# Kernel tuning notes

Hardware: AMD Instinct MI355X
Metric: run time of the kernel (lower is better)

Reference implementation:

```python
import jax, jax.numpy as jnp
import numpy as np

FRAME_T = 8
NUM_K = 10


def _masked_att(att, temp):
    # att: [B, H, P, P] -> softmax over groups of size P//FRAME_T, top-k threshold mask
    B, H, P, _ = att.shape
    D = P // FRAME_T
    a = att.reshape(B, H, P, FRAME_T, D)
    a = jax.nn.softmax(a / temp, axis=-1)
    # k-th largest value per row as threshold (torch.topk values are sorted desc)
    margin = jax.lax.top_k(a, NUM_K)[0][..., -1]  # [B,H,P,FRAME_T]
    a = a * (a >= margin[..., None])
    return a  # [B,H,P,FRAME_T,D]


def setup_inputs() -> dict:
    key = jax.random.key(0)
    k1, k2, k3, k4 = jax.random.split(key, 4)
    B, H, P, hd = 4, 12, 1568, 64
    return {
        "att_s": jax.random.normal(k1, (B, H, P, P), dtype=jnp.float32),
        "att_t": jax.random.normal(k2, (B, H, P, P), dtype=jnp.float32),
        "v_s": jax.random.normal(k3, (B, H, P, hd), dtype=jnp.float32),
        "v_t": jax.random.normal(k4, (B, H, P, hd), dtype=jnp.float32),
    }


def reference(att_s, att_t, v_s, v_t):
    temp = jnp.float32(1.0)
    B, H, P, _ = att_t.shape
    H_s = att_s.shape[1]
    h_dim = v_t.shape[-1]
    D = P // FRAME_T

    a_s = _masked_att(att_s, temp)  # [B,Hs,P,T,D]
    a_t = _masked_att(att_t, temp)  # [B,H,P,T,D]

    vt = v_t.reshape(B, H, D, FRAME_T, h_dim)
    vs = v_s.reshape(B, H_s, D, FRAME_T, h_dim)

    norm_s = a_s.sum(-1)  # [B,Hs,P,T]
    norm_t = a_t.sum(-1)

    o_s = jnp.einsum('bhptd,bhdte->bhpte', a_s, vs) / norm_s[..., None]
    o_t = jnp.einsum('bhptd,bhdte->bhpte', a_t, vt) / norm_t[..., None]

    loss = jnp.mean((o_s - o_t) ** 2)
    return loss
```

## Files before the change

kernel.cpp:

```cpp
#include <hip/hip_runtime.h>
#include <hip/hip_bf16.h>

#define PP 1568
#define TT 8
#define DD 196
#define HD 64
#define NBH 48
#define NROW (NBH*PP*TT)
#define RPW 32
#define WPB 2
#define NWAVE (NROW/RPW)
#define NBLK5 (NWAVE/WPB)
#define NXCD 8
#define CPX (NBLK5/NXCD)
#define NPART NWAVE
#define NRED1 ((NPART+255)/256)
#define SUB (8*DD*4)
#define VSLAB (DD*TT*HD)
#define WPBH 392
#define KMASK 0xFFFFFF00u
#define NEG_INF (-3.0e38f)

typedef float f4 __attribute__((ext_vector_type(4)));
typedef unsigned u4v __attribute__((ext_vector_type(4)));

__device__ __forceinline__ float readlane_f(float v, int l) {
    return __int_as_float(__builtin_amdgcn_readlane(__float_as_int(v), l));
}

__device__ __forceinline__ float wave_sum_u(float v) {
#define STEPS(ctrl) { float t_ = __int_as_float(__builtin_amdgcn_update_dpp( \
        0, __float_as_int(v), ctrl, 0xF, 0xF, true)); v += t_; }
    STEPS(0x111) STEPS(0x112) STEPS(0x114) STEPS(0x118) STEPS(0x142) STEPS(0x143)
#undef STEPS
    return readlane_f(v, 63);
}

__device__ __forceinline__ float kval(float k) {
    return __uint_as_float(__float_as_uint(k) & KMASK);
}

struct K6  { float k0,k1,k2,k3,k4,k5; };
struct K10 { float k0,k1,k2,k3,k4,k5,k6,k7,k8,k9; };
struct MR  { K10 f; float mx; };

#define PUTK6(Q,X,D) { \
  unsigned cu_=(__float_as_uint(X)&KMASK)|(unsigned)(D); \
  float c_=__uint_as_float(cu_); \
  float n0_=fmaxf(Q.k0,c_); \
  float n1_=__builtin_amdgcn_fmed3f(Q.k0,Q.k1,c_); \
  float n2_=__builtin_amdgcn_fmed3f(Q.k1,Q.k2,c_); \
  float n3_=__builtin_amdgcn_fmed3f(Q.k2,Q.k3,c_); \
  float n4_=__builtin_amdgcn_fmed3f(Q.k3,Q.k4,c_); \
  float n5_=__builtin_amdgcn_fmed3f(Q.k4,Q.k5,c_); \
  Q.k0=n0_; Q.k1=n1_; Q.k2=n2_; Q.k3=n3_; Q.k4=n4_; Q.k5=n5_; }
#define PUT4K6(Q,V,D0) PUTK6(Q,(V).x,(D0)) PUTK6(Q,(V).y,(D0)+1) \
                       PUTK6(Q,(V).z,(D0)+2) PUTK6(Q,(V).w,(D0)+3)

__device__ __forceinline__ K6 chain_rows(const char* stg, int a, int b8) {
    K6 q = {NEG_INF,NEG_INF,NEG_INF,NEG_INF,NEG_INF,NEG_INF};
    const char* rb = stg + a*784 + b8*16;
    f4 v;
    v = *(const f4*)(rb);       PUT4K6(q, v, b8*4)
    v = *(const f4*)(rb+128);   PUT4K6(q, v, b8*4+32)
    v = *(const f4*)(rb+256);   PUT4K6(q, v, b8*4+64)
    v = *(const f4*)(rb+384);   PUT4K6(q, v, b8*4+96)
    v = *(const f4*)(rb+512);   PUT4K6(q, v, b8*4+128)
    v = *(const f4*)(rb+640);   PUT4K6(q, v, b8*4+160)
    if (b8 == 7) { f4 w = *(const f4*)(stg + a*784 + 768); PUT4K6(q, w, 192) }
    return q;
}

#define FSWZ(x, pat) __int_as_float(__builtin_amdgcn_ds_swizzle(__float_as_int(x), pat))
__device__ __forceinline__ K6 kshuf8_6(K6 a) {
    K6 r;
    r.k0=FSWZ(a.k0,0x201F); r.k1=FSWZ(a.k1,0x201F); r.k2=FSWZ(a.k2,0x201F);
    r.k3=FSWZ(a.k3,0x201F); r.k4=FSWZ(a.k4,0x201F); r.k5=FSWZ(a.k5,0x201F);
    return r;
}
__device__ __forceinline__ K10 kshuf16(K10 a) {
    K10 r;
    r.k0=FSWZ(a.k0,0x401F); r.k1=FSWZ(a.k1,0x401F); r.k2=FSWZ(a.k2,0x401F);
    r.k3=FSWZ(a.k3,0x401F); r.k4=FSWZ(a.k4,0x401F); r.k5=FSWZ(a.k5,0x401F);
    r.k6=FSWZ(a.k6,0x401F); r.k7=FSWZ(a.k7,0x401F); r.k8=FSWZ(a.k8,0x401F);
    r.k9=FSWZ(a.k9,0x401F);
    return r;
}
__device__ __forceinline__ float fbp(int bpx, float x) {
    return __int_as_float(__builtin_amdgcn_ds_bpermute(bpx, __float_as_int(x)));
}
__device__ __forceinline__ K10 kbp32(K10 a, int bpx) {
    K10 r;
    r.k0=fbp(bpx,a.k0); r.k1=fbp(bpx,a.k1); r.k2=fbp(bpx,a.k2);
    r.k3=fbp(bpx,a.k3); r.k4=fbp(bpx,a.k4); r.k5=fbp(bpx,a.k5);
    r.k6=fbp(bpx,a.k6); r.k7=fbp(bpx,a.k7); r.k8=fbp(bpx,a.k8);
    r.k9=fbp(bpx,a.k9);
    return r;
}

__device__ __forceinline__ K10 kmrg66(K6 A, K6 B) {
    float p00=fminf(A.k0,B.k0);
    float p01=fminf(A.k0,B.k1), p10=fminf(A.k1,B.k0);
    float p02=fminf(A.k0,B.k2), p11=fminf(A.k1,B.k1), p20=fminf(A.k2,B.k0);
    float p03=fminf(A.k0,B.k3), p12=fminf(A.k1,B.k2), p21=fminf(A.k2,B.k1), p30=fminf(A.k3,B.k0);
    float p04=fminf(A.k0,B.k4), p13=fminf(A.k1,B.k3), p22=fminf(A.k2,B.k2), p31=fminf(A.k3,B.k1), p40=fminf(A.k4,B.k0);
    float p05=fminf(A.k0,B.k5), p14=fminf(A.k1,B.k4), p23=fminf(A.k2,B.k3), p32=fminf(A.k3,B.k2), p41=fminf(A.k4,B.k1), p50=fminf(A.k5,B.k0);
    float p15=fminf(A.k1,B.k5), p24=fminf(A.k2,B.k4), p33=fminf(A.k3,B.k3), p42=fminf(A.k4,B.k2), p51=fminf(A.k5,B.k1);
    float p25=fminf(A.k2,B.k5), p34=fminf(A.k3,B.k4), p43=fminf(A.k4,B.k3), p52=fminf(A.k5,B.k2);
    float p35=fminf(A.k3,B.k5), p44=fminf(A.k4,B.k4), p53=fminf(A.k5,B.k3);
    K10 M;
    M.k0=fmaxf(A.k0,B.k0);
    M.k1=fmaxf(fmaxf(A.k1,B.k1),p00);
    M.k2=fmaxf(fmaxf(A.k2,B.k2),fmaxf(p01,p10));
    M.k3=fmaxf(fmaxf(A.k3,B.k3),fmaxf(p02,fmaxf(p11,p20)));
    M.k4=fmaxf(fmaxf(A.k4,B.k4),fmaxf(fmaxf(p03,p12),fmaxf(p21,p30)));
    M.k5=fmaxf(fmaxf(A.k5,B.k5),fmaxf(fmaxf(p04,p13),fmaxf(p22,fmaxf(p31,p40))));
    M.k6=fmaxf(fmaxf(p05,p14),fmaxf(fmaxf(p23,p32),fmaxf(p41,p50)));
    M.k7=fmaxf(fmaxf(p15,p24),fmaxf(p33,fmaxf(p42,p51)));
    M.k8=fmaxf(fmaxf(p25,p34),fmaxf(p43,p52));
    M.k9=fmaxf(p35,fmaxf(p44,p53));
    return M;
}

__device__ __forceinline__ K10 kmrg(K10 A, K10 B) {
    float p00=fminf(A.k0,B.k0);
    float p01=fminf(A.k0,B.k1), p10=fminf(A.k1,B.k0);
    float p02=fminf(A.k0,B.k2), p11=fminf(A.k1,B.k1), p20=fminf(A.k2,B.k0);
    float p03=fminf(A.k0,B.k3), p12=fminf(A.k1,B.k2), p21=fminf(A.k2,B.k1), p30=fminf(A.k3,B.k0);
    float p04=fminf(A.k0,B.k4), p13=fminf(A.k1,B.k3), p22=fminf(A.k2,B.k2), p31=fminf(A.k3,B.k1), p40=fminf(A.k4,B.k0);
    float p05=fminf(A.k0,B.k5), p14=fminf(A.k1,B.k4), p23=fminf(A.k2,B.k3), p32=fminf(A.k3,B.k2), p41=fminf(A.k4,B.k1), p50=fminf(A.k5,B.k0);
    float p06=fminf(A.k0,B.k6), p15=fminf(A.k1,B.k5), p24=fminf(A.k2,B.k4), p33=fminf(A.k3,B.k3), p42=fminf(A.k4,B.k2), p51=fminf(A.k5,B.k1), p60=fminf(A.k6,B.k0);
    float p07=fminf(A.k0,B.k7), p16=fminf(A.k1,B.k6), p25=fminf(A.k2,B.k5), p34=fminf(A.k3,B.k4), p43=fminf(A.k4,B.k3), p52=fminf(A.k5,B.k2), p61=fminf(A.k6,B.k1), p70=fminf(A.k7,B.k0);
    float p08=fminf(A.k0,B.k8), p17=fminf(A.k1,B.k7), p26=fminf(A.k2,B.k6), p35=fminf(A.k3,B.k5), p44=fminf(A.k4,B.k4), p53=fminf(A.k5,B.k3), p62=fminf(A.k6,B.k2), p71=fminf(A.k7,B.k1), p80=fminf(A.k8,B.k0);
    K10 M;
    M.k0=fmaxf(A.k0,B.k0);
    M.k1=fmaxf(fmaxf(A.k1,B.k1),p00);
    M.k2=fmaxf(fmaxf(A.k2,B.k2),fmaxf(p01,p10));
    M.k3=fmaxf(fmaxf(A.k3,B.k3),fmaxf(p02,fmaxf(p11,p20)));
    M.k4=fmaxf(fmaxf(A.k4,B.k4),fmaxf(fmaxf(p03,p12),fmaxf(p21,p30)));
    M.k5=fmaxf(fmaxf(A.k5,B.k5),fmaxf(fmaxf(p04,p13),fmaxf(p22,fmaxf(p31,p40))));
    M.k6=fmaxf(fmaxf(A.k6,B.k6),fmaxf(fmaxf(p05,p14),fmaxf(fmaxf(p23,p32),fmaxf(p41,p50))));
    M.k7=fmaxf(fmaxf(A.k7,B.k7),fmaxf(fmaxf(fmaxf(p06,p15),fmaxf(p24,p33)),fmaxf(fmaxf(p42,p51),p60)));
    M.k8=fmaxf(fmaxf(A.k8,B.k8),fmaxf(fmaxf(fmaxf(p07,p16),fmaxf(p25,p34)),fmaxf(fmaxf(p43,p52),fmaxf(p61,p70))));
    M.k9=fmaxf(fmaxf(A.k9,B.k9),fmaxf(fmaxf(fmaxf(p08,p17),fmaxf(p26,p35)),fmaxf(fmaxf(p44,p53),fmaxf(fmaxf(p62,p71),p80))));
    return M;
}

__device__ __forceinline__ MR merge_all(K6 q, int bpx) {
    K10 m = kmrg66(q, kshuf8_6(q));
    K10 n = kmrg(m, kshuf16(m));
    K10 r = kbp32(n, bpx);
    MR out;
    out.mx = fmaxf(n.k0, r.k0);
    out.f.k0=fmaxf(n.k0,r.k9); out.f.k1=fmaxf(n.k1,r.k8); out.f.k2=fmaxf(n.k2,r.k7);
    out.f.k3=fmaxf(n.k3,r.k6); out.f.k4=fmaxf(n.k4,r.k5); out.f.k5=fmaxf(n.k5,r.k4);
    out.f.k6=fmaxf(n.k6,r.k3); out.f.k7=fmaxf(n.k7,r.k2); out.f.k8=fmaxf(n.k8,r.k1);
    out.f.k9=fmaxf(n.k9,r.k0);
    return out;
}

#define LOADR(R, P) { const char* p_=(P); \
    R##0=*(const f4*)(p_+lane*16); \
    R##1=*(const f4*)(p_+1024+lane*16); \
    R##2=*(const f4*)(p_+2048+lane*16); \
    R##3=*(const f4*)(p_+3072+lane*16); \
    R##4=*(const f4*)(p_+4096+lane*16); \
    R##5=*(const f4*)(p_+5120+lane*16); \
    if (lane<8) R##6=*(const f4*)(p_+6144+lane*16); }
#define STORER(R) { \
    *(f4*)(stg+lane*16)=R##0; *(f4*)(stg+1024+lane*16)=R##1; \
    *(f4*)(stg+2048+lane*16)=R##2; *(f4*)(stg+3072+lane*16)=R##3; \
    *(f4*)(stg+4096+lane*16)=R##4; *(f4*)(stg+5120+lane*16)=R##5; \
    if (lane<8) *(f4*)(stg+6144+lane*16)=R##6; }

#define PKW(F,K) ((__float_as_uint(F)&KMASK)|(__float_as_uint(K)&0xFFu))

__global__ __launch_bounds__(128) void vtop_main(
        const float* __restrict__ att_s, const float* __restrict__ att_t,
        const float* __restrict__ v_s,   const float* __restrict__ v_t,
        float* __restrict__ partial) {
    __shared__ f4  stgv[WPB][SUB/16];
    __shared__ u4v wbuf[WPB][5][RPW];

    int tid  = threadIdx.x;
    int wid  = tid >> 6;
    int lane = tid & 63;
    char* stg = (char*)&stgv[wid][0];
    int a = lane & 7, b8 = lane >> 3;
    int bpx = (lane ^ 32) << 2;

    int blk = (blockIdx.x % NXCD) * CPX + blockIdx.x / NXCD;
    int gwave = blk * WPB + wid;
    int bh = gwave / WPBH;

    const char* baseS = (const char*)att_s + (size_t)gwave * (RPW*DD*4);
    const char* baseT = (const char*)att_t + (size_t)gwave * (RPW*DD*4);

    f4 rs0{},rs1{},rs2{},rs3{},rs4{},rs5{},rs6{};
    f4 rt0{},rt1{},rt2{},rt3{},rt4{},rt5{},rt6{};

    LOADR(rs, baseS)

#pragma unroll 1
    for (int s = 0; s < 4; ++s) {
        STORER(rs)
        LOADR(rt, baseT + s*SUB)
        K6 qS = chain_rows(stg, a, b8);
        MR mS = merge_all(qS, bpx);
        STORER(rt)
        if (s < 3) LOADR(rs, baseS + (s+1)*SUB)
        K6 qT = chain_rows(stg, a, b8);
        MR mT = merge_all(qT, bpx);
        K10 fS = mS.f, fT = mT.f;

        float CS = kval(mS.mx), CT = kval(mT.mx);
        float wS0=__expf(kval(fS.k0)-CS), wS1=__expf(kval(fS.k1)-CS),
              wS2=__expf(kval(fS.k2)-CS), wS3=__expf(kval(fS.k3)-CS),
              wS4=__expf(kval(fS.k4)-CS), wS5=__expf(kval(fS.k5)-CS),
              wS6=__expf(kval(fS.k6)-CS), wS7=__expf(kval(fS.k7)-CS),
              wS8=__expf(kval(fS.k8)-CS), wS9=__expf(kval(fS.k9)-CS);
        float wT0=__expf(kval(fT.k0)-CT), wT1=__expf(kval(fT.k1)-CT),
              wT2=__expf(kval(fT.k2)-CT), wT3=__expf(kval(fT.k3)-CT),
              wT4=__expf(kval(fT.k4)-CT), wT5=__expf(kval(fT.k5)-CT),
              wT6=__expf(kval(fT.k6)-CT), wT7=__expf(kval(fT.k7)-CT),
              wT8=__expf(kval(fT.k8)-CT), wT9=__expf(kval(fT.k9)-CT);
        float wsS = (((wS0+wS1)+(wS2+wS3))+((wS4+wS5)+(wS6+wS7)))+(wS8+wS9);
        float wsT = (((wT0+wT1)+(wT2+wT3))+((wT4+wT5)+(wT6+wT7)))+(wT8+wT9);
        float invS =  __builtin_amdgcn_rcpf(wsS);
        float invT = -__builtin_amdgcn_rcpf(wsT);

        if (lane < 8) {
            int row = (s << 3) | lane;
            u4v w;
            w.x=PKW(wS0*invS,fS.k0); w.y=PKW(wS1*invS,fS.k1);
            w.z=PKW(wS2*invS,fS.k2); w.w=PKW(wS3*invS,fS.k3);
            wbuf[wid][0][row]=w;
            w.x=PKW(wS4*invS,fS.k4); w.y=PKW(wS5*invS,fS.k5);
            w.z=PKW(wS6*invS,fS.k6); w.w=PKW(wS7*invS,fS.k7);
            wbuf[wid][1][row]=w;
            w.x=PKW(wS8*invS,fS.k8); w.y=PKW(wS9*invS,fS.k9);
            w.z=PKW(wT0*invT,fT.k0); w.w=PKW(wT1*invT,fT.k1);
            wbuf[wid][2][row]=w;
            w.x=PKW(wT2*invT,fT.k2); w.y=PKW(wT3*invT,fT.k3);
            w.z=PKW(wT4*invT,fT.k4); w.w=PKW(wT5*invT,fT.k5);
            wbuf[wid][3][row]=w;
            w.x=PKW(wT6*invT,fT.k6); w.y=PKW(wT7*invT,fT.k7);
            w.z=PKW(wT8*invT,fT.k8); w.w=PKW(wT9*invT,fT.k9);
            wbuf[wid][4][row]=w;
        }
    }

    const float* vSb = v_s + (size_t)bh * VSLAB;
    const float* vTb = v_t + (size_t)bh * VSLAB;
    unsigned ul = (unsigned)lane;
    float lacc = 0.f;
#pragma unroll 1
    for (int k = 0; k < RPW; ++k) {
        unsigned t64 = ((unsigned)(k & 7) << 6);
        const float* vSk = vSb + t64;
        const float* vTk = vTb + t64;
        u4v w0v=wbuf[wid][0][k], w1v=wbuf[wid][1][k], w2v=wbuf[wid][2][k],
            w3v=wbuf[wid][3][k], w4v=wbuf[wid][4][k];
        float d0=0.f, d1=0.f, d2=0.f, d3=0.f;
#define TRM(U, VB, ACC) { unsigned pk_=(unsigned)__builtin_amdgcn_readfirstlane((int)(U)); \
        float wf_ = __uint_as_float(pk_ & KMASK); \
        ACC = fmaf(wf_, VB[((pk_ & 0xFFu) << 9) + ul], ACC); }
        TRM(w0v.x, vSk, d0) TRM(w0v.y, vSk, d1) TRM(w0v.z, vSk, d2) TRM(w0v.w, vSk, d3)
        TRM(w1v.x, vSk, d0) TRM(w1v.y, vSk, d1) TRM(w1v.z, vSk, d2) TRM(w1v.w, vSk, d3)
        TRM(w2v.x, vSk, d0) TRM(w2v.y, vSk, d1)
        TRM(w2v.z, vTk, d2) TRM(w2v.w, vTk, d3)
        TRM(w3v.x, vTk, d0) TRM(w3v.y, vTk, d1) TRM(w3v.z, vTk, d2) TRM(w3v.w, vTk, d3)
        TRM(w4v.x, vTk, d0) TRM(w4v.y, vTk, d1) TRM(w4v.z, vTk, d2) TRM(w4v.w, vTk, d3)
#undef TRM
        float dsum = (d0 + d1) + (d2 + d3);
        lacc = fmaf(dsum, dsum, lacc);
    }

    float tot = wave_sum_u(lacc);
    if (lane == 0) partial[gwave] = tot;
}

__global__ __launch_bounds__(256) void vtop_reduce1(
        const float* __restrict__ partial, float* __restrict__ p2) {
    int i = blockIdx.x * 256 + threadIdx.x;
    float v = (i < NPART) ? partial[i] : 0.f;
    float wtot = wave_sum_u(v);
    __shared__ float sm[4];
    int lane = threadIdx.x & 63, wid = threadIdx.x >> 6;
    if (lane == 0) sm[wid] = wtot;
    __syncthreads();
    if (threadIdx.x == 0) p2[blockIdx.x] = (sm[0] + sm[1]) + (sm[2] + sm[3]);
}

__global__ __launch_bounds__(256) void vtop_reduce2(
        const float* __restrict__ p2, float* __restrict__ out) {
    __shared__ double smd[256];
    double a = 0.0;
    if (threadIdx.x < NRED1) a = (double)p2[threadIdx.x];
    smd[threadIdx.x] = a;
    __syncthreads();
    for (int s = 128; s > 0; s >>= 1) {
        if (threadIdx.x < s) smd[threadIdx.x] += smd[threadIdx.x + s];
        __syncthreads();
    }
    if (threadIdx.x == 0) {
        const double inv_n = 1.0 / ((double)NBH * PP * TT * HD);
        out[0] = (float)(smd[0] * inv_n);
    }
}

extern "C" void kernel_launch(void* const* d_in, const int* in_sizes, int n_in,
                              void* d_out, int out_size, void* d_ws, size_t ws_size,
                              hipStream_t stream) {
    const float* att_s = (const float*)d_in[0];
    const float* att_t = (const float*)d_in[1];
    const float* v_s   = (const float*)d_in[2];
    const float* v_t   = (const float*)d_in[3];
    float* out     = (float*)d_out;
    float* partial = (float*)d_ws;
    float* p2      = (float*)d_ws + NPART;

    vtop_main<<<NBLK5, 128, 0, stream>>>(att_s, att_t, v_s, v_t, partial);
    vtop_reduce1<<<NRED1, 256, 0, stream>>>(partial, p2);
    vtop_reduce2<<<1, 256, 0, stream>>>(p2, out);
}
```

Baseline: 323.7 us.

## Stage attention rows with direct global-to-LDS loads instead of register copies

Replaces the register-held prefetch of each row block (global load into VGPRs, then store to LDS) with `global_load_lds` builtins that write straight into the per-wave staging buffer. A `vmcnt(0)` wait precedes each read of the buffer. The loop is reordered so the S-side softmax weights are computed while the T-side block is in flight, and the next S block is issued after the T rows are read. This drops the register round trip and 28 f4 prefetch registers, which may help occupancy. In exchange only one block is in flight at a time, and overwriting the single buffer right after `chain_rows` relies on the LDS reads finishing before the async writes land.

```diff
diff --git a/kernel.cpp b/kernel.cpp
--- a/kernel.cpp
+++ b/kernel.cpp
@@ -38,6 +38,12 @@
 
 __device__ __forceinline__ float kval(float k) {
     return __uint_as_float(__float_as_uint(k) & KMASK);
+}
+
+__device__ __forceinline__ void gload_lds(const void* g, void* l) {
+    __builtin_amdgcn_global_load_lds(
+        (const __attribute__((address_space(1))) unsigned*)g,
+        (__attribute__((address_space(3))) unsigned*)l, 16, 0, 0);
 }
 
 struct K6  { float k0,k1,k2,k3,k4,k5; };
@@ -159,19 +165,15 @@
     return out;
 }
 
-#define LOADR(R, P) { const char* p_=(P); \
-    R##0=*(const f4*)(p_+lane*16); \
-    R##1=*(const f4*)(p_+1024+lane*16); \
-    R##2=*(const f4*)(p_+2048+lane*16); \
-    R##3=*(const f4*)(p_+3072+lane*16); \
-    R##4=*(const f4*)(p_+4096+lane*16); \
-    R##5=*(const f4*)(p_+5120+lane*16); \
-    if (lane<8) R##6=*(const f4*)(p_+6144+lane*16); }
-#define STORER(R) { \
-    *(f4*)(stg+lane*16)=R##0; *(f4*)(stg+1024+lane*16)=R##1; \
-    *(f4*)(stg+2048+lane*16)=R##2; *(f4*)(stg+3072+lane*16)=R##3; \
-    *(f4*)(stg+4096+lane*16)=R##4; *(f4*)(stg+5120+lane*16)=R##5; \
-    if (lane<8) *(f4*)(stg+6144+lane*16)=R##6; }
+#define STAGE(SRC) { const char* s_=(SRC); \
+    gload_lds(s_ +         (size_t)lane*16, stg); \
+    gload_lds(s_ + 1024 +  (size_t)lane*16, stg+1024); \
+    gload_lds(s_ + 2048 +  (size_t)lane*16, stg+2048); \
+    gload_lds(s_ + 3072 +  (size_t)lane*16, stg+3072); \
+    gload_lds(s_ + 4096 +  (size_t)lane*16, stg+4096); \
+    gload_lds(s_ + 5120 +  (size_t)lane*16, stg+5120); \
+    if (lane < 8) gload_lds(s_ + 6144 + (size_t)lane*16, stg+6144); }
+#define WAITV asm volatile("s_waitcnt vmcnt(0)" ::: "memory");
 
 #define PKW(F,K) ((__float_as_uint(F)&KMASK)|(__float_as_uint(K)&0xFFu))
 
@@ -196,37 +198,36 @@
     const char* baseS = (const char*)att_s + (size_t)gwave * (RPW*DD*4);
     const char* baseT = (const char*)att_t + (size_t)gwave * (RPW*DD*4);
 
-    f4 rs0{},rs1{},rs2{},rs3{},rs4{},rs5{},rs6{};
-    f4 rt0{},rt1{},rt2{},rt3{},rt4{},rt5{},rt6{};
-
-    LOADR(rs, baseS)
+    STAGE(baseS)
 
 #pragma unroll 1
     for (int s = 0; s < 4; ++s) {
-        STORER(rs)
-        LOADR(rt, baseT + s*SUB)
+        WAITV
         K6 qS = chain_rows(stg, a, b8);
+        STAGE(baseT + s*SUB)
         MR mS = merge_all(qS, bpx);
-        STORER(rt)
-        if (s < 3) LOADR(rs, baseS + (s+1)*SUB)
-        K6 qT = chain_rows(stg, a, b8);
-        MR mT = merge_all(qT, bpx);
-        K10 fS = mS.f, fT = mT.f;
-
-        float CS = kval(mS.mx), CT = kval(mT.mx);
+        K10 fS = mS.f;
+        float CS = kval(mS.mx);
         float wS0=__expf(kval(fS.k0)-CS), wS1=__expf(kval(fS.k1)-CS),
               wS2=__expf(kval(fS.k2)-CS), wS3=__expf(kval(fS.k3)-CS),
               wS4=__expf(kval(fS.k4)-CS), wS5=__expf(kval(fS.k5)-CS),
               wS6=__expf(kval(fS.k6)-CS), wS7=__expf(kval(fS.k7)-CS),
               wS8=__expf(kval(fS.k8)-CS), wS9=__expf(kval(fS.k9)-CS);
+        float wsS = (((wS0+wS1)+(wS2+wS3))+((wS4+wS5)+(wS6+wS7)))+(wS8+wS9);
+        float invS = __builtin_amdgcn_rcpf(wsS);
+
+        WAITV
+        K6 qT = chain_rows(stg, a, b8);
+        if (s < 3) STAGE(baseS + (s+1)*SUB)
+        MR mT = merge_all(qT, bpx);
+        K10 fT = mT.f;
+        float CT = kval(mT.mx);
         float wT0=__expf(kval(fT.k0)-CT), wT1=__expf(kval(fT.k1)-CT),
               wT2=__expf(kval(fT.k2)-CT), wT3=__expf(kval(fT.k3)-CT),
               wT4=__expf(kval(fT.k4)-CT), wT5=__expf(kval(fT.k5)-CT),
               wT6=__expf(kval(fT.k6)-CT), wT7=__expf(kval(fT.k7)-CT),
               wT8=__expf(kval(fT.k8)-CT), wT9=__expf(kval(fT.k9)-CT);
-        float wsS = (((wS0+wS1)+(wS2+wS3))+((wS4+wS5)+(wS6+wS7)))+(wS8+wS9);
         float wsT = (((wT0+wT1)+(wT2+wT3))+((wT4+wT5)+(wT6+wT7)))+(wT8+wT9);
-        float invS =  __builtin_amdgcn_rcpf(wsS);
         float invT = -__builtin_amdgcn_rcpf(wsT);
 
         if (lane < 8) {
```

Result: no change. 323.0 us (-0.2%).
